# Kernel optimization log

Measured on AMD Instinct MI355X. Metric: run time of the kernel, lower is better.

The kernel has to match this reference:

```python
import jax, jax.numpy as jnp
import numpy as np


def setup_inputs() -> dict:
    key = jax.random.key(0)
    k1, k2, k3 = jax.random.split(key, 3)
    B, T, D = 128, 128, 512
    return {
        "input_real": jax.random.normal(k1, (B, T, D), dtype=jnp.float32),
        "input_imag": jax.random.normal(k2, (B, T, D), dtype=jnp.float32),
        "weight": jax.random.uniform(k3, (B, T), dtype=jnp.float32),
    }


def reference(input_real, input_imag, weight):
    # weighted sum over the sequence dim T: [B,T,D] * [B,T,1] -> sum -> [B,D]
    w = weight[:, :, None]
    out_r = jnp.sum(input_real * w, axis=1)  # [B, D]
    out_i = jnp.sum(input_imag * w, axis=1)  # [B, D]
    # complex rank-1 outer products: [B,D,1] x [B,1,D] -> [B,D,D]
    rr = jnp.einsum('bi,bj->bij', out_r, out_r)
    ii = jnp.einsum('bi,bj->bij', out_i, out_i)
    ir = jnp.einsum('bi,bj->bij', out_i, out_r)
    ri = jnp.einsum('bi,bj->bij', out_r, out_i)
    output_r = rr + ii  # real part of |psi><psi|
    output_i = ir - ri  # imag part
    return (output_r, output_i)
```

## Files before the change

kernel.cpp:

```cpp
#include <hip/hip_runtime.h>


#define B_  128
#define T_  128
#define D_  512
#define D4_ 128

typedef float f32x4 __attribute__((ext_vector_type(4)));

__global__ __launch_bounds__(256)
void reduce_kernel(const f32x4* __restrict__ xr,
                   const f32x4* __restrict__ xi,
                   const float* __restrict__ w,
                   f32x4* __restrict__ outr,
                   f32x4* __restrict__ outi)
{
    const int b     = blockIdx.y;
    const int chunk = blockIdx.x;
    const int tid   = threadIdx.x;
    const int c     = tid & 31;
    const int g     = tid >> 5;
    const int d4    = chunk * 32 + c;

    __shared__ float ws[T_];
    if (tid < T_) ws[tid] = w[b * T_ + tid];
    __syncthreads();

    float wreg[16];
    #pragma unroll
    for (int k = 0; k < 16; ++k) wreg[k] = ws[g * 16 + k];

    const f32x4* br = xr + ((size_t)b * T_ + g * 16) * D4_ + d4;
    const f32x4* bm = xi + ((size_t)b * T_ + g * 16) * D4_ + d4;

    f32x4 ar = (f32x4)0.f;
    f32x4 ai = (f32x4)0.f;

    #pragma unroll
    for (int k = 0; k < 16; ++k) {
        const f32x4 r = br[k * D4_];
        const f32x4 m = bm[k * D4_];
        const float wt = wreg[k];
        ar += r * wt;
        ai += m * wt;
    }

    __shared__ __align__(16) f32x4 pr[8][32];
    __shared__ __align__(16) f32x4 pi[8][32];
    pr[g][c] = ar;
    pi[g][c] = ai;
    __syncthreads();

    if (g == 0) {
        #pragma unroll
        for (int k = 1; k < 8; ++k) {
            ar += pr[k][c];
            ai += pi[k][c];
        }
        outr[b * D4_ + d4] = ar;
        outi[b * D4_ + d4] = ai;
    }
}

#define ROWS_ 16

__global__ __launch_bounds__(256)
void outer_kernel(const f32x4* __restrict__ our4,
                  const f32x4* __restrict__ oui4,
                  f32x4* __restrict__ outR,
                  f32x4* __restrict__ outI)
{
    const int b     = blockIdx.y;
    const int chunk = blockIdx.x;
    const int tid   = threadIdx.x;

    __shared__ __align__(16) f32x4 s4r[D4_];
    __shared__ __align__(16) f32x4 s4i[D4_];
    if (tid < 128) s4r[tid]       = our4[b * D4_ + tid];
    else           s4i[tid - 128] = oui4[b * D4_ + (tid - 128)];
    __syncthreads();

    const int j4   = tid & (D4_ - 1);
    const int isub = tid >> 7;

    const f32x4 rj = s4r[j4];
    const f32x4 ij = s4i[j4];
    const float* sr = (const float*)s4r;
    const float* si = (const float*)s4i;

    float ri[ROWS_ / 2], mi[ROWS_ / 2];
    #pragma unroll
    for (int r = 0; r < ROWS_ / 2; ++r) {
        const int i = chunk * ROWS_ + 2 * r + isub;
        ri[r] = sr[i];
        mi[r] = si[i];
    }

    const size_t base = ((size_t)b * D_ + (size_t)chunk * ROWS_) * D4_ + j4;

    #pragma unroll
    for (int r = 0; r < ROWS_ / 2; ++r) {
        const float a = ri[r];
        const float m = mi[r];

        const f32x4 oR = a * rj + m * ij;
        const f32x4 oI = m * rj - a * ij;

        const size_t off = base + (size_t)(2 * r + isub) * D4_;
        __builtin_nontemporal_store(oR, &outR[off]);
        __builtin_nontemporal_store(oI, &outI[off]);
    }
}

extern "C" void kernel_launch(void* const* d_in, const int* in_sizes, int n_in,
                              void* d_out, int out_size, void* d_ws, size_t ws_size,
                              hipStream_t stream) {
    const float* xr = (const float*)d_in[0];
    const float* xi = (const float*)d_in[1];
    const float* w  = (const float*)d_in[2];

    float* out = (float*)d_out;
    float* our = (float*)d_ws;
    float* oui = our + B_ * D_;

    reduce_kernel<<<dim3(4, B_), 256, 0, stream>>>(
        (const f32x4*)xr, (const f32x4*)xi, w,
        (f32x4*)our, (f32x4*)oui);

    outer_kernel<<<dim3(32, B_), 256, 0, stream>>>(
        (const f32x4*)our, (const f32x4*)oui,
        (f32x4*)out,
        (f32x4*)(out + (size_t)B_ * D_ * D_));
}
```

Measured before the change: 313.3 us.

## Fuse weighted reduction and outer product into one kernel per batch half

Merges the sequence reduction and the complex outer-product kernels into a single kernel. Each block redundantly recomputes the reduced vector for its batch and then writes half of the DxD outputs, which removes the intermediate workspace round trip and one launch. Grid shrinks to 256 blocks of 512 threads, each writing 256 rows in a loop, so parallelism and latency hiding may drop. Nontemporal stores are also replaced by plain stores. The input reads double because both halves recompute the same reduction.

```diff
diff --git a/kernel.cpp b/kernel.cpp
--- a/kernel.cpp
+++ b/kernel.cpp
@@ -8,107 +8,77 @@
 
 typedef float f32x4 __attribute__((ext_vector_type(4)));
 
-__global__ __launch_bounds__(256)
-void reduce_kernel(const f32x4* __restrict__ xr,
-                   const f32x4* __restrict__ xi,
-                   const float* __restrict__ w,
-                   f32x4* __restrict__ outr,
-                   f32x4* __restrict__ outi)
+__global__ __launch_bounds__(512)
+void fused_kernel(const f32x4* __restrict__ xr,
+                  const f32x4* __restrict__ xi,
+                  const float* __restrict__ w,
+                  f32x4* __restrict__ outR,
+                  f32x4* __restrict__ outI)
 {
-    const int b     = blockIdx.y;
-    const int chunk = blockIdx.x;
-    const int tid   = threadIdx.x;
-    const int c     = tid & 31;
-    const int g     = tid >> 5;
-    const int d4    = chunk * 32 + c;
+    const int b    = blockIdx.y;
+    const int half = blockIdx.x;
+    const int tid  = threadIdx.x;
+    const int c    = tid & (D4_ - 1);
+    const int q    = tid >> 7;
 
     __shared__ float ws[T_];
     if (tid < T_) ws[tid] = w[b * T_ + tid];
     __syncthreads();
 
-    float wreg[16];
+    float wreg[32];
     #pragma unroll
-    for (int k = 0; k < 16; ++k) wreg[k] = ws[g * 16 + k];
+    for (int k = 0; k < 32; ++k) wreg[k] = ws[q * 32 + k];
 
-    const f32x4* br = xr + ((size_t)b * T_ + g * 16) * D4_ + d4;
-    const f32x4* bm = xi + ((size_t)b * T_ + g * 16) * D4_ + d4;
+    const f32x4* br = xr + ((size_t)b * T_ + q * 32) * D4_ + c;
+    const f32x4* bm = xi + ((size_t)b * T_ + q * 32) * D4_ + c;
 
     f32x4 ar = (f32x4)0.f;
     f32x4 ai = (f32x4)0.f;
-
     #pragma unroll
-    for (int k = 0; k < 16; ++k) {
-        const f32x4 r = br[k * D4_];
-        const f32x4 m = bm[k * D4_];
-        const float wt = wreg[k];
-        ar += r * wt;
-        ai += m * wt;
+    for (int k = 0; k < 32; ++k) {
+        ar += br[k * D4_] * wreg[k];
+        ai += bm[k * D4_] * wreg[k];
     }
 
-    __shared__ __align__(16) f32x4 pr[8][32];
-    __shared__ __align__(16) f32x4 pi[8][32];
-    pr[g][c] = ar;
-    pi[g][c] = ai;
+    __shared__ __align__(16) f32x4 pr[4][D4_];
+    __shared__ __align__(16) f32x4 pi[4][D4_];
+    pr[q][c] = ar;
+    pi[q][c] = ai;
     __syncthreads();
 
-    if (g == 0) {
+    __shared__ __align__(16) f32x4 sor4[D4_];
+    __shared__ __align__(16) f32x4 soi4[D4_];
+    if (q == 0) {
         #pragma unroll
-        for (int k = 1; k < 8; ++k) {
-            ar += pr[k][c];
-            ai += pi[k][c];
-        }
-        outr[b * D4_ + d4] = ar;
-        outi[b * D4_ + d4] = ai;
+        for (int k = 1; k < 4; ++k) { ar += pr[k][c]; ai += pi[k][c]; }
+        sor4[c] = ar;
+        soi4[c] = ai;
     }
-}
-
-#define ROWS_ 16
-
-__global__ __launch_bounds__(256)
-void outer_kernel(const f32x4* __restrict__ our4,
-                  const f32x4* __restrict__ oui4,
-                  f32x4* __restrict__ outR,
-                  f32x4* __restrict__ outI)
-{
-    const int b     = blockIdx.y;
-    const int chunk = blockIdx.x;
-    const int tid   = threadIdx.x;
-
-    __shared__ __align__(16) f32x4 s4r[D4_];
-    __shared__ __align__(16) f32x4 s4i[D4_];
-    if (tid < 128) s4r[tid]       = our4[b * D4_ + tid];
-    else           s4i[tid - 128] = oui4[b * D4_ + (tid - 128)];
     __syncthreads();
 
     const int j4   = tid & (D4_ - 1);
     const int isub = tid >> 7;
 
-    const f32x4 rj = s4r[j4];
-    const f32x4 ij = s4i[j4];
-    const float* sr = (const float*)s4r;
-    const float* si = (const float*)s4i;
+    const f32x4 rj = sor4[j4];
+    const f32x4 ij = soi4[j4];
+    const float* sor = (const float*)sor4;
+    const float* soi = (const float*)soi4;
 
-    float ri[ROWS_ / 2], mi[ROWS_ / 2];
-    #pragma unroll
-    for (int r = 0; r < ROWS_ / 2; ++r) {
-        const int i = chunk * ROWS_ + 2 * r + isub;
-        ri[r] = sr[i];
-        mi[r] = si[i];
-    }
+    const int i0 = half * (D_ / 2);
+    f32x4* __restrict__ pR = outR + ((size_t)b * D_ + i0) * D4_ + j4;
+    f32x4* __restrict__ pI = outI + ((size_t)b * D_ + i0) * D4_ + j4;
 
-    const size_t base = ((size_t)b * D_ + (size_t)chunk * ROWS_) * D4_ + j4;
-
-    #pragma unroll
-    for (int r = 0; r < ROWS_ / 2; ++r) {
-        const float a = ri[r];
-        const float m = mi[r];
+    #pragma unroll 8
+    for (int r = 0; r < D_ / 2 / 4; ++r) {
+        const int   row = r * 4 + isub;
+        const float a = sor[i0 + row];
+        const float m = soi[i0 + row];
 
         const f32x4 oR = a * rj + m * ij;
         const f32x4 oI = m * rj - a * ij;
 
-        const size_t off = base + (size_t)(2 * r + isub) * D4_;
-        __builtin_nontemporal_store(oR, &outR[off]);
-        __builtin_nontemporal_store(oI, &outI[off]);
+        pR[(size_t)row * D4_] = oR;
+        pI[(size_t)row * D4_] = oI;
     }
 }
 
@@ -120,15 +90,9 @@
     const float* w  = (const float*)d_in[2];
 
     float* out = (float*)d_out;
-    float* our = (float*)d_ws;
-    float* oui = our + B_ * D_;
 
-    reduce_kernel<<<dim3(4, B_), 256, 0, stream>>>(
+    fused_kernel<<<dim3(2, B_), 512, 0, stream>>>(
         (const f32x4*)xr, (const f32x4*)xi, w,
-        (f32x4*)our, (f32x4*)oui);
-
-    outer_kernel<<<dim3(32, B_), 256, 0, stream>>>(
-        (const f32x4*)our, (const f32x4*)oui,
         (f32x4*)out,
         (f32x4*)(out + (size_t)B_ * D_ * D_));
 }
```

Measured after the change: 315.9 us. About the same (+0.8%).
